# Optimization experiments

Hardware: AMD Instinct MI355X
Metric: run time of the kernel (lower is better)

## Reference

```python
import jax, jax.numpy as jnp
import numpy as np

PS = 2      # patch_size
TOPK = 3    # topk


def setup_inputs() -> dict:
    key = jax.random.key(0)
    x = jax.random.normal(key, (8, 128, 64, 64), dtype=jnp.float32)
    alpha = jnp.asarray(5.0, dtype=jnp.float32)  # nn.Parameter alpha
    return {"x": x, "alpha": alpha}


def _forward(x, alpha):
    ps = PS
    b, c, h, w = x.shape
    nph, npw = h // ps, w // ps
    npatch = nph * npw
    pa = ps * ps
    # F.normalize(p=2, dim=-3) with torch eps=1e-12
    norm = jnp.maximum(jnp.sqrt(jnp.sum(x * x, axis=1, keepdims=True)), 1e-12)
    x = x / norm
    # patchify -> [b, c, npatch, patch_area] (patches h-major, pixels row-major)
    xp = x.reshape(b, c, nph, ps, npw, ps).transpose(0, 1, 2, 4, 3, 5)
    xp = xp.reshape(b, c, npatch, pa)
    diag_idx = jnp.arange(ps) * (ps + 1)  # [0, 3] for ps=2
    # gather diagonal pixels of each patch -> [b, ps, npatch, c]
    xd = xp[:, :, :, diag_idx].transpose(0, 3, 2, 1)
    # patch correlation matmul -> [b, ps, npatch, npatch]
    corr = jnp.einsum('bpnc,bpmc->bpnm', xd, xd)
    avg = jnp.mean(corr, axis=1, keepdims=True)
    s = jnp.concatenate([corr, avg], axis=1)  # [b, ps+1, npatch, npatch]
    # ZeroWindow gaussian mask (rat_s=0.05); channel index = patch center (r,c)
    sr, sc = 0.05 * nph, 0.05 * npw
    rr = jnp.arange(nph, dtype=jnp.float32)
    cc = jnp.arange(npw, dtype=jnp.float32)
    cent_r, cent_c = jnp.meshgrid(rr, cc, indexing='ij')
    cent_r = cent_r.reshape(npatch)
    cent_c = cent_c.reshape(npatch)
    gr = jnp.exp(-(rr[None, :] - cent_r[:, None]) ** 2 / (2.0 * sr * sr))  # [npatch, nph]
    gc = jnp.exp(-(cc[None, :] - cent_c[:, None]) ** 2 / (2.0 * sc * sc))  # [npatch, npw]
    mask = (1.0 - gr[:, :, None] * gc[:, None, :]).reshape(npatch, npatch)
    s = s * mask[None, None]
    a = s * alpha
    # double (row + col) softmax
    s = jax.nn.softmax(a, axis=-1) * jax.nn.softmax(a, axis=-2)
    # expand avg channel to all patch pixels, scatter diagonal channels back
    new_x = jnp.broadcast_to(s[:, -1:], (b, pa, npatch, npatch))
    new_x = new_x.at[:, diag_idx].set(s[:, :ps])
    # un-patchify second npatch axis to spatial [b, npatch, h, w]
    y = jnp.swapaxes(new_x, 1, 3)  # [b, npatch, npatch, pa]
    y = y.reshape(b, npatch, nph, npw, ps, ps).transpose(0, 1, 2, 4, 3, 5)
    y = y.reshape(b, npatch, h, w)
    # topk over the npatch axis (dim=-3)
    vals = jax.lax.top_k(jnp.moveaxis(y, 1, -1), TOPK)[0]  # [b, h, w, k]
    return jnp.moveaxis(vals, -1, 1)  # [b, k, h, w]


def reference(x, alpha):
    return _forward(x, alpha)
```

## Files before the change

### kernel.cpp

```cpp
#include <hip/hip_runtime.h>
#include <hip/hip_bf16.h>
#include <math.h>

#define NB 8
#define NC 128
#define NH 64
#define NW 64
#define NP 1024
#define TWO_SIG2 5.12f
#define LOG2E 1.44269504089f

static const size_t PSUM_OFF_B = 0;
static const size_t PBUF_OFF_B = (size_t)NB * 3 * 4 * NP * 4;
static const size_t XD_OFF_B   = PBUF_OFF_B + (size_t)NB * NP * 3 * 4 * 3 * 4;

typedef __bf16 bf16x8 __attribute__((ext_vector_type(8)));
typedef float f32x4 __attribute__((ext_vector_type(4)));

__device__ __forceinline__ int iabs_(int v) { return v < 0 ? -v : v; }

#define INSERT3(v, A, Bq, Cq)                          \
  {                                                    \
    const float _na = fmaxf(A, (v));                   \
    const float _nb = __builtin_amdgcn_fmed3f(A, Bq, (v)); \
    Cq = __builtin_amdgcn_fmed3f(Bq, Cq, (v));         \
    A = _na;                                           \
    Bq = _nb;                                          \
  }

#define MERGE3(a0, a1, a2, b0, b1, b2)       \
  {                                          \
    const float _x1 = fmaxf(a0, b0);         \
    const float _y1 = fminf(a0, b0);         \
    const float _x2 = fmaxf(a1, b1);         \
    const float _z  = fmaxf(a2, b2);         \
    a0 = _x1;                                \
    a1 = fmaxf(_y1, _x2);                    \
    a2 = fmaxf(fminf(_y1, _x2), _z);         \
  }

__global__ __launch_bounds__(256) void k1_norm(const float* __restrict__ x,
                                               __hip_bfloat16* __restrict__ xd) {
  __shared__ __align__(16) float tile[NC * 65];
  const int chunk = blockIdx.x;
  const int p = blockIdx.y;
  const int b = blockIdx.z;
  const int t = threadIdx.x;
  const int pix = t & 63;
  const int cw = t >> 6;
  const int nbase = chunk * 64;

  {
    const int n = nbase + pix;
    const int i = ((n >> 5) << 1) + p;
    const int jf = (n & 31);
    const float* xb = x + (size_t)b * NC * NH * NW + (size_t)i * NW;
    for (int cc = 0; cc < 32; ++cc) {
      const int c = (cc << 2) + cw;
      const float2 v2 = ((const float2*)(xb + (size_t)c * NH * NW))[jf];
      tile[c * 65 + pix] = (p == 0) ? v2.x : v2.y;
    }
  }
  __syncthreads();

  const int lane = t & 63;
  const int w = t >> 6;
  for (int pg = 0; pg < 16; ++pg) {
    const int pixel = (pg << 2) + w;
    const float v0 = tile[lane * 65 + pixel];
    const float v1 = tile[(lane + 64) * 65 + pixel];
    float ss = v0 * v0 + v1 * v1;
#pragma unroll
    for (int m = 32; m >= 1; m >>= 1) ss += __shfl_xor(ss, m, 64);
    const float inv = 1.0f / fmaxf(sqrtf(ss), 1e-12f);
    __hip_bfloat16* xr = xd + ((size_t)((b * 2 + p) * NP) + nbase + pixel) * NC;
    xr[lane] = __float2bfloat16(v0 * inv);
    xr[lane + 64] = __float2bfloat16(v1 * inv);
  }
}

__global__ __launch_bounds__(256) void k2_sums(const ushort* __restrict__ xd,
                                               const float* __restrict__ alpha_p,
                                               float* __restrict__ psum) {
  __shared__ __align__(16) __bf16 As[2][64 * 136];
  __shared__ __align__(16) __bf16 Bs[2][64 * 136];
  __shared__ float er[32];
  __shared__ float erA[32];
  const int t = threadIdx.x;
  const float K = (*alpha_p) * LOG2E;
  if (t < 32) {
    const float e = __expf(-(float)(t * t) / TWO_SIG2);
    er[t] = e;
    erA[t] = K * e;
  }

  const int cchunk = blockIdx.x;
  const int rowtile = blockIdx.y;
  const int b = blockIdx.z;
  const int i0 = rowtile << 6;
  const int jb = cchunk << 8;

#pragma unroll
  for (int pl = 0; pl < 2; ++pl) {
    const float4* ga = (const float4*)(xd + ((size_t)(b * 2 + pl) * NP + i0) * NC);
#pragma unroll
    for (int it = 0; it < 4; ++it) {
      const int f = (it << 8) + t;
      const int r = f >> 4, q = f & 15;
      *(float4*)(&As[pl][r * 136 + q * 8]) = ga[f];
    }
  }

  const int wave = t >> 6;
  const int lane = t & 63;
  const int lrow = lane & 15;
  const int kq = lane >> 4;

  float sums[3][4];
#pragma unroll
  for (int ch = 0; ch < 3; ++ch)
#pragma unroll
    for (int reg = 0; reg < 4; ++reg) sums[ch][reg] = 0.f;

  for (int sc = 0; sc < 4; ++sc) {
    const int j0 = jb + (sc << 6);
    __syncthreads();
#pragma unroll
    for (int pl = 0; pl < 2; ++pl) {
      const float4* gb = (const float4*)(xd + ((size_t)(b * 2 + pl) * NP + j0) * NC);
#pragma unroll
      for (int it = 0; it < 4; ++it) {
        const int f = (it << 8) + t;
        const int r = f >> 4, q = f & 15;
        *(float4*)(&Bs[pl][r * 136 + q * 8]) = gb[f];
      }
    }
    __syncthreads();

    f32x4 acc[2][4];
#pragma unroll
    for (int pl = 0; pl < 2; ++pl)
#pragma unroll
      for (int ct = 0; ct < 4; ++ct)
#pragma unroll
        for (int u = 0; u < 4; ++u) acc[pl][ct][u] = 0.f;

#pragma unroll
    for (int kc = 0; kc < 4; ++kc) {
      const int kk = kc * 32 + (kq << 3);
      const bf16x8 a0 = *(const bf16x8*)(&As[0][(wave * 16 + lrow) * 136 + kk]);
      const bf16x8 a1 = *(const bf16x8*)(&As[1][(wave * 16 + lrow) * 136 + kk]);
#pragma unroll
      for (int ct = 0; ct < 4; ++ct) {
        const bf16x8 b0 = *(const bf16x8*)(&Bs[0][(ct * 16 + lrow) * 136 + kk]);
        const bf16x8 b1 = *(const bf16x8*)(&Bs[1][(ct * 16 + lrow) * 136 + kk]);
        acc[0][ct] = __builtin_amdgcn_mfma_f32_16x16x32_bf16(a0, b0, acc[0][ct], 0, 0, 0);
        acc[1][ct] = __builtin_amdgcn_mfma_f32_16x16x32_bf16(a1, b1, acc[1][ct], 0, 0, 0);
      }
    }

#pragma unroll
    for (int ct = 0; ct < 4; ++ct) {
      const int m = j0 + ct * 16 + lrow;
      const int rm = m >> 5, cm = m & 31;
#pragma unroll
      for (int reg = 0; reg < 4; ++reg) {
        const int n = i0 + wave * 16 + kq * 4 + reg;
        const int rn = n >> 5, cn = n & 31;
        const float fm2 = fmaf(-erA[iabs_(rn - rm)], er[iabs_(cn - cm)], K);
        const float g0 = fm2 * acc[0][ct][reg];
        const float g1 = fm2 * acc[1][ct][reg];
        sums[0][reg] += exp2f(g0);
        sums[1][reg] += exp2f(g1);
        sums[2][reg] += exp2f(0.5f * (g0 + g1));
      }
    }
  }

#pragma unroll
  for (int off = 1; off < 16; off <<= 1)
#pragma unroll
    for (int ch = 0; ch < 3; ++ch)
#pragma unroll
      for (int reg = 0; reg < 4; ++reg)
        sums[ch][reg] += __shfl_xor(sums[ch][reg], off, 64);

  if (lrow == 0) {
#pragma unroll
    for (int ch = 0; ch < 3; ++ch)
#pragma unroll
      for (int reg = 0; reg < 4; ++reg) {
        const int n = i0 + wave * 16 + kq * 4 + reg;
        psum[(((size_t)b * 3 + ch) * 4 + cchunk) * NP + n] = sums[ch][reg];
      }
  }
}

__global__ __launch_bounds__(256) void k4_topk(const ushort* __restrict__ xd,
                                               const float* __restrict__ alpha_p,
                                               const float* __restrict__ psum,
                                               float* __restrict__ pbuf) {
  __shared__ __align__(16) __bf16 As[2][64 * 136];
  __shared__ __align__(16) __bf16 Bs[2][64 * 136];
  __shared__ float er[32];
  __shared__ float erA[32];
  __shared__ float rsr[3][64];
  __shared__ float rsc[3][256];
  const int t = threadIdx.x;
  const float K = (*alpha_p) * LOG2E;
  if (t < 32) {
    const float e = __expf(-(float)(t * t) / TWO_SIG2);
    er[t] = e;
    erA[t] = K * e;
  }

  const int cchunk = blockIdx.x;
  const int rowtile = blockIdx.y;
  const int b = blockIdx.z;
  const int i0 = rowtile << 6;
  const int jb = cchunk << 8;

  if (t < 192) {
    const int ch = t >> 6, r = t & 63;
    const float* pp = psum + ((size_t)b * 3 + ch) * 4 * NP + i0 + r;
    rsr[ch][r] = 1.0f / (pp[0] + pp[NP] + pp[2 * NP] + pp[3 * NP]);
  }
#pragma unroll
  for (int ch = 0; ch < 3; ++ch) {
    const float* pp = psum + ((size_t)b * 3 + ch) * 4 * NP + jb + t;
    rsc[ch][t] = 1.0f / (pp[0] + pp[NP] + pp[2 * NP] + pp[3 * NP]);
  }

#pragma unroll
  for (int pl = 0; pl < 2; ++pl) {
    const float4* ga = (const float4*)(xd + ((size_t)(b * 2 + pl) * NP + i0) * NC);
#pragma unroll
    for (int it = 0; it < 4; ++it) {
      const int f = (it << 8) + t;
      const int r = f >> 4, q = f & 15;
      *(float4*)(&As[pl][r * 136 + q * 8]) = ga[f];
    }
  }

  const int wave = t >> 6;
  const int lane = t & 63;
  const int lrow = lane & 15;
  const int kq = lane >> 4;

  float tA[3][4], tB[3][4], tC[3][4];
#pragma unroll
  for (int ch = 0; ch < 3; ++ch)
#pragma unroll
    for (int reg = 0; reg < 4; ++reg) { tA[ch][reg] = 0.f; tB[ch][reg] = 0.f; tC[ch][reg] = 0.f; }

  for (int sc = 0; sc < 4; ++sc) {
    const int j0 = jb + (sc << 6);
    __syncthreads();
#pragma unroll
    for (int pl = 0; pl < 2; ++pl) {
      const float4* gb = (const float4*)(xd + ((size_t)(b * 2 + pl) * NP + j0) * NC);
#pragma unroll
      for (int it = 0; it < 4; ++it) {
        const int f = (it << 8) + t;
        const int r = f >> 4, q = f & 15;
        *(float4*)(&Bs[pl][r * 136 + q * 8]) = gb[f];
      }
    }
    __syncthreads();

    f32x4 acc[2][4];
#pragma unroll
    for (int pl = 0; pl < 2; ++pl)
#pragma unroll
      for (int ct = 0; ct < 4; ++ct)
#pragma unroll
        for (int u = 0; u < 4; ++u) acc[pl][ct][u] = 0.f;

#pragma unroll
    for (int kc = 0; kc < 4; ++kc) {
      const int kk = kc * 32 + (kq << 3);
      const bf16x8 a0 = *(const bf16x8*)(&As[0][(wave * 16 + lrow) * 136 + kk]);
      const bf16x8 a1 = *(const bf16x8*)(&As[1][(wave * 16 + lrow) * 136 + kk]);
#pragma unroll
      for (int ct = 0; ct < 4; ++ct) {
        const bf16x8 b0 = *(const bf16x8*)(&Bs[0][(ct * 16 + lrow) * 136 + kk]);
        const bf16x8 b1 = *(const bf16x8*)(&Bs[1][(ct * 16 + lrow) * 136 + kk]);
        acc[0][ct] = __builtin_amdgcn_mfma_f32_16x16x32_bf16(a0, b0, acc[0][ct], 0, 0, 0);
        acc[1][ct] = __builtin_amdgcn_mfma_f32_16x16x32_bf16(a1, b1, acc[1][ct], 0, 0, 0);
      }
    }

#pragma unroll
    for (int ct = 0; ct < 4; ++ct) {
      const int mc = sc * 64 + ct * 16 + lrow;
      const int m = jb + mc;
      const int rm = m >> 5, cm = m & 31;
      const float im0 = rsc[0][mc], im1 = rsc[1][mc], im2 = rsc[2][mc];
#pragma unroll
      for (int reg = 0; reg < 4; ++reg) {
        const int nr = wave * 16 + kq * 4 + reg;
        const int n = i0 + nr;
        const int rn = n >> 5, cn = n & 31;
        const float fm2 = fmaf(-erA[iabs_(rn - rm)], er[iabs_(cn - cm)], K);
        const float g0 = fm2 * acc[0][ct][reg];
        const float g1 = fm2 * acc[1][ct][reg];
        const float e0 = exp2f(g0);
        const float e1 = exp2f(g1);
        const float e2 = exp2f(0.5f * (g0 + g1));
        const float q0 = e0 * e0 * im0;
        const float q1 = e1 * e1 * im1;
        const float q2 = e2 * e2 * im2;
        INSERT3(q0, tA[0][reg], tB[0][reg], tC[0][reg]);
        INSERT3(q1, tA[1][reg], tB[1][reg], tC[1][reg]);
        INSERT3(q2, tA[2][reg], tB[2][reg], tC[2][reg]);
      }
    }
  }

#pragma unroll
  for (int off = 1; off < 16; off <<= 1)
#pragma unroll
    for (int ch = 0; ch < 3; ++ch)
#pragma unroll
      for (int reg = 0; reg < 4; ++reg) {
        const float b0 = __shfl_xor(tA[ch][reg], off, 64);
        const float b1 = __shfl_xor(tB[ch][reg], off, 64);
        const float b2 = __shfl_xor(tC[ch][reg], off, 64);
        MERGE3(tA[ch][reg], tB[ch][reg], tC[ch][reg], b0, b1, b2);
      }

  if (lrow == 0) {
#pragma unroll
    for (int ch = 0; ch < 3; ++ch)
#pragma unroll
      for (int reg = 0; reg < 4; ++reg) {
        const int nr = wave * 16 + kq * 4 + reg;
        const int n = i0 + nr;
        const float irn = rsr[ch][nr];
        const size_t base = ((((size_t)b * NP + n) * 3 + ch) * 4 + cchunk) * 3;
        pbuf[base + 0] = tA[ch][reg] * irn;
        pbuf[base + 1] = tB[ch][reg] * irn;
        pbuf[base + 2] = tC[ch][reg] * irn;
      }
  }
}

__global__ __launch_bounds__(256) void k5_merge(const float* __restrict__ pbuf,
                                                float* __restrict__ out) {
  const int tau = blockIdx.x * 256 + threadIdx.x;
  const int b = tau >> 10;
  const int n = tau & (NP - 1);
  const int rn = n >> 5, cn = n & 31;

  float f0[3], f1[3], f2[3];
#pragma unroll
  for (int ch = 0; ch < 3; ++ch) {
    const size_t base = (((size_t)tau * 3 + ch) * 4) * 3;
    f0[ch] = pbuf[base + 0];
    f1[ch] = pbuf[base + 1];
    f2[ch] = pbuf[base + 2];
#pragma unroll
    for (int p = 1; p < 4; ++p) {
      const float b0 = pbuf[base + p * 3 + 0];
      const float b1 = pbuf[base + p * 3 + 1];
      const float b2 = pbuf[base + p * 3 + 2];
      MERGE3(f0[ch], f1[ch], f2[ch], b0, b1, b2);
    }
  }

  float* ob = out + (size_t)b * 3 * (NH * NW);
  const int i00 = ((rn << 1) * NW) + (cn << 1);
#pragma unroll
  for (int tt = 0; tt < 3; ++tt) {
    float* op = ob + (size_t)tt * (NH * NW);
    const float r0 = (tt == 0) ? f0[0] : (tt == 1) ? f1[0] : f2[0];
    const float r1 = (tt == 0) ? f0[1] : (tt == 1) ? f1[1] : f2[1];
    const float r2 = (tt == 0) ? f0[2] : (tt == 1) ? f1[2] : f2[2];
    op[i00] = r0;
    op[i00 + NW + 1] = r1;
    op[i00 + 1] = r2;
    op[i00 + NW] = r2;
  }
}

extern "C" void kernel_launch(void* const* d_in, const int* in_sizes, int n_in,
                              void* d_out, int out_size, void* d_ws, size_t ws_size,
                              hipStream_t stream) {
  const float* x = (const float*)d_in[0];
  const float* alpha = (const float*)d_in[1];
  float* out = (float*)d_out;
  char* ws = (char*)d_ws;

  float* psum = (float*)(ws + PSUM_OFF_B);
  float* pbuf = (float*)(ws + PBUF_OFF_B);
  __hip_bfloat16* xd = (__hip_bfloat16*)(ws + XD_OFF_B);

  k1_norm<<<dim3(16, 2, NB), 256, 0, stream>>>(x, xd);
  k2_sums<<<dim3(4, 16, NB), 256, 0, stream>>>((const ushort*)xd, alpha, psum);
  k4_topk<<<dim3(4, 16, NB), 256, 0, stream>>>((const ushort*)xd, alpha, psum, pbuf);
  k5_merge<<<dim3(32), 256, 0, stream>>>(pbuf, out);
}
```

Measured before the change: 111.5 us.

## Fold top-k merge into k4 via last-block atomic counter; reuse exps for avg channel

Removes the separate k5_merge launch. Each row tile of k4 now increments an atomic counter, which k2 resets beforehand, and the last of its four column-chunk blocks merges the partial top-3 lists and writes the output. Separately, the avg-channel exponential is computed as e0*e1 instead of a third exp2, which is algebraically identical and saves one transcendental per element. The fusion adds threadfences and an atomic per block, and leaves the final merge serialized in the last-arriving block.

```diff
diff --git a/kernel.cpp b/kernel.cpp
--- a/kernel.cpp
+++ b/kernel.cpp
@@ -12,7 +12,8 @@
 
 static const size_t PSUM_OFF_B = 0;
 static const size_t PBUF_OFF_B = (size_t)NB * 3 * 4 * NP * 4;
-static const size_t XD_OFF_B   = PBUF_OFF_B + (size_t)NB * NP * 3 * 4 * 3 * 4;
+static const size_t CNT_OFF_B  = PBUF_OFF_B + (size_t)NB * NP * 3 * 4 * 3 * 4;
+static const size_t XD_OFF_B   = CNT_OFF_B + 1024;
 
 typedef __bf16 bf16x8 __attribute__((ext_vector_type(8)));
 typedef float f32x4 __attribute__((ext_vector_type(4)));
@@ -81,7 +82,8 @@
 
 __global__ __launch_bounds__(256) void k2_sums(const ushort* __restrict__ xd,
                                                const float* __restrict__ alpha_p,
-                                               float* __restrict__ psum) {
+                                               float* __restrict__ psum,
+                                               int* __restrict__ cnt) {
   __shared__ __align__(16) __bf16 As[2][64 * 136];
   __shared__ __align__(16) __bf16 Bs[2][64 * 136];
   __shared__ float er[32];
@@ -100,6 +102,8 @@
   const int i0 = rowtile << 6;
   const int jb = cchunk << 8;
 
+  if (cchunk == 0 && t == 0) cnt[b * 16 + rowtile] = 0;
+
 #pragma unroll
   for (int pl = 0; pl < 2; ++pl) {
     const float4* ga = (const float4*)(xd + ((size_t)(b * 2 + pl) * NP + i0) * NC);
@@ -199,13 +203,16 @@
 __global__ __launch_bounds__(256) void k4_topk(const ushort* __restrict__ xd,
                                                const float* __restrict__ alpha_p,
                                                const float* __restrict__ psum,
-                                               float* __restrict__ pbuf) {
+                                               float* __restrict__ pbuf,
+                                               int* __restrict__ cnt,
+                                               float* __restrict__ out) {
   __shared__ __align__(16) __bf16 As[2][64 * 136];
   __shared__ __align__(16) __bf16 Bs[2][64 * 136];
   __shared__ float er[32];
   __shared__ float erA[32];
   __shared__ float rsr[3][64];
   __shared__ float rsc[3][256];
+  __shared__ int lastFlag;
   const int t = threadIdx.x;
   const float K = (*alpha_p) * LOG2E;
   if (t < 32) {
@@ -306,10 +313,9 @@
         const float g1 = fm2 * acc[1][ct][reg];
         const float e0 = exp2f(g0);
         const float e1 = exp2f(g1);
-        const float e2 = exp2f(0.5f * (g0 + g1));
         const float q0 = e0 * e0 * im0;
         const float q1 = e1 * e1 * im1;
-        const float q2 = e2 * e2 * im2;
+        const float q2 = e0 * e1 * im2;
         INSERT3(q0, tA[0][reg], tB[0][reg], tC[0][reg]);
         INSERT3(q1, tA[1][reg], tB[1][reg], tC[1][reg]);
         INSERT3(q2, tA[2][reg], tB[2][reg], tC[2][reg]);
@@ -343,43 +349,44 @@
         pbuf[base + 2] = tC[ch][reg] * irn;
       }
   }
-}
-
-__global__ __launch_bounds__(256) void k5_merge(const float* __restrict__ pbuf,
-                                                float* __restrict__ out) {
-  const int tau = blockIdx.x * 256 + threadIdx.x;
-  const int b = tau >> 10;
-  const int n = tau & (NP - 1);
-  const int rn = n >> 5, cn = n & 31;
-
-  float f0[3], f1[3], f2[3];
-#pragma unroll
-  for (int ch = 0; ch < 3; ++ch) {
-    const size_t base = (((size_t)tau * 3 + ch) * 4) * 3;
-    f0[ch] = pbuf[base + 0];
-    f1[ch] = pbuf[base + 1];
-    f2[ch] = pbuf[base + 2];
+
+  __threadfence();
+  __syncthreads();
+  if (t == 0) lastFlag = (atomicAdd(&cnt[b * 16 + rowtile], 1) == 3);
+  __syncthreads();
+  if (!lastFlag) return;
+  __threadfence();
+
+  if (t < 192) {
+    const int r = t & 63;
+    const int ch = t >> 6;
+    const int n = i0 + r;
+    const size_t base = (((size_t)b * NP + n) * 3 + ch) * 4 * 3;
+    float f0 = pbuf[base + 0], f1 = pbuf[base + 1], f2 = pbuf[base + 2];
 #pragma unroll
     for (int p = 1; p < 4; ++p) {
       const float b0 = pbuf[base + p * 3 + 0];
       const float b1 = pbuf[base + p * 3 + 1];
       const float b2 = pbuf[base + p * 3 + 2];
-      MERGE3(f0[ch], f1[ch], f2[ch], b0, b1, b2);
-    }
-  }
-
-  float* ob = out + (size_t)b * 3 * (NH * NW);
-  const int i00 = ((rn << 1) * NW) + (cn << 1);
-#pragma unroll
-  for (int tt = 0; tt < 3; ++tt) {
-    float* op = ob + (size_t)tt * (NH * NW);
-    const float r0 = (tt == 0) ? f0[0] : (tt == 1) ? f1[0] : f2[0];
-    const float r1 = (tt == 0) ? f0[1] : (tt == 1) ? f1[1] : f2[1];
-    const float r2 = (tt == 0) ? f0[2] : (tt == 1) ? f1[2] : f2[2];
-    op[i00] = r0;
-    op[i00 + NW + 1] = r1;
-    op[i00 + 1] = r2;
-    op[i00 + NW] = r2;
+      MERGE3(f0, f1, f2, b0, b1, b2);
+    }
+
+    const int rn = n >> 5, cn = n & 31;
+    float* ob = out + (size_t)b * 3 * (NH * NW);
+    const int i00 = ((rn << 1) * NW) + (cn << 1);
+    const float v[3] = {f0, f1, f2};
+#pragma unroll
+    for (int tt = 0; tt < 3; ++tt) {
+      float* op = ob + (size_t)tt * (NH * NW);
+      if (ch == 0) {
+        op[i00] = v[tt];
+      } else if (ch == 1) {
+        op[i00 + NW + 1] = v[tt];
+      } else {
+        op[i00 + 1] = v[tt];
+        op[i00 + NW] = v[tt];
+      }
+    }
   }
 }
 
@@ -393,10 +400,10 @@
 
   float* psum = (float*)(ws + PSUM_OFF_B);
   float* pbuf = (float*)(ws + PBUF_OFF_B);
+  int* cnt = (int*)(ws + CNT_OFF_B);
   __hip_bfloat16* xd = (__hip_bfloat16*)(ws + XD_OFF_B);
 
   k1_norm<<<dim3(16, 2, NB), 256, 0, stream>>>(x, xd);
-  k2_sums<<<dim3(4, 16, NB), 256, 0, stream>>>((const ushort*)xd, alpha, psum);
-  k4_topk<<<dim3(4, 16, NB), 256, 0, stream>>>((const ushort*)xd, alpha, psum, pbuf);
-  k5_merge<<<dim3(32), 256, 0, stream>>>(pbuf, out);
+  k2_sums<<<dim3(4, 16, NB), 256, 0, stream>>>((const ushort*)xd, alpha, psum, cnt);
+  k4_topk<<<dim3(4, 16, NB), 256, 0, stream>>>((const ushort*)xd, alpha, psum, pbuf, cnt, out);
 }
```

New measurement: 175.8 us. 1.58x slower.
